# Kernel optimization log

Hardware: AMD Instinct MI355X
Metric: run time of the kernel (lower is better)

Reference implementation:

```python
import jax, jax.numpy as jnp
import numpy as np

B, A, T, D, H, NB, OUT = 64, 128, 6, 256, 512, 5, 401
ALPHA = 0.5
BETA = 0.5


def _lin_init(key, n_in, n_out, extra=()):
    bound = 1.0 / np.sqrt(n_in)
    kw, kb = jax.random.split(key)
    W = jax.random.uniform(kw, extra + (n_in, n_out), minval=-bound, maxval=bound, dtype=jnp.float32)
    b = jax.random.uniform(kb, extra + (n_out,), minval=-bound, maxval=bound, dtype=jnp.float32)
    return W, b


def setup_inputs() -> dict:
    key = jax.random.key(0)
    ks = jax.random.split(key, 8)
    stdv = 1.0 / np.sqrt(D)
    anchor = jax.random.uniform(ks[0], (1, 1, T, D), minval=-stdv, maxval=stdv, dtype=jnp.float32)
    sW1, sb1 = _lin_init(ks[1], D, D, (NB,))
    sW2, sb2 = _lin_init(ks[2], D, D, (NB,))
    cW1, cb1 = _lin_init(ks[3], D, D, (NB,))
    cW2, cb2 = _lin_init(ks[4], D, D, (NB,))
    dW1, db1 = _lin_init(ks[5], D, H)
    dW2, db2 = _lin_init(ks[6], H, OUT)
    final_embedding = jax.random.normal(ks[7], (B, A, D), dtype=jnp.float32)
    return {"final_embedding": final_embedding, "anchor": anchor,
            "sW1": sW1, "sb1": sb1, "sW2": sW2, "sb2": sb2,
            "cW1": cW1, "cb1": cb1, "cW2": cW2, "cb2": cb2,
            "dW1": dW1, "db1": db1, "dW2": dW2, "db2": db2}


def _mlp2(x, W1, b1, W2, b2):
    # 2-layer MLP (Linear -> ReLU -> Linear), applied to last dim
    return jax.nn.relu(x @ W1 + b1) @ W2 + b2


def reference(final_embedding, anchor, sW1, sb1, sW2, sb2, cW1, cb1, cW2, cb2, dW1, db1, dW2, db2):
    b, a = final_embedding.shape[:2]
    # s: [B, A, T, D] repeated anchors; c: [B, A, 1, D] context
    s = jnp.broadcast_to(anchor, (b, a, T, D))
    c = final_embedding[:, :, None, :]
    for i in range(NB):
        s_new = _mlp2(s, sW1[i], sb1[i], sW2[i], sb2[i])
        c_new = _mlp2(c, cW1[i], cb1[i], cW2[i], cb2[i])
        s_new = s_new * c_new                      # gate, broadcasts over T
        agg_c = jnp.max(s_new, axis=-2, keepdims=True)
        s = ALPHA * s + BETA * s_new               # sliding running mean
        c = ALPHA * c + BETA * agg_c
    # decoder MLP on trajectory embeddings s: [B, A, T, D]
    res = jax.nn.relu(s @ dW1 + db1) @ dW2 + db2   # [B, A, T, 401]
    coordinates = res[..., :160].reshape(b, a, T, 80, 2)
    av = res[..., 160:240].reshape(b, a, T, 80, 1)
    bv = res[..., 240:320].reshape(b, a, T, 80, 1)
    cv = res[..., 320:400].reshape(b, a, T, 80, 1)
    probas = res[..., -1]                          # [B, A, T]
    cov = jnp.concatenate([jnp.exp(av) * jnp.cosh(bv), jnp.sinh(bv),
                           jnp.sinh(bv), jnp.exp(-av) * jnp.cosh(bv)], axis=-1) * jnp.exp(cv)
    covariance_matrices = cov.reshape(b, a, T, 80, 2, 2)
    return (probas, coordinates, covariance_matrices)
```

## Files before the change

kernel.cpp:

```cpp
#include <hip/hip_runtime.h>
#include <math.h>


constexpr int Tn  = 6;
constexpr int Dn  = 256;
constexpr int Hn  = 512;
constexpr int NBn = 5;
constexpr int OUTn = 401;
constexpr int BA  = 8192;
constexpr int MR  = 49152;
constexpr float kAlpha = 0.5f;
constexpr float kBeta  = 0.5f;

typedef __bf16 bf16_8 __attribute__((ext_vector_type(8)));
typedef float  f32x4  __attribute__((ext_vector_type(4)));

__device__ __forceinline__ void async_copy16(const __bf16* g, __bf16* l) {
  __builtin_amdgcn_global_load_lds(
      (const __attribute__((address_space(1))) void*)g,
      (__attribute__((address_space(3))) void*)l, 16, 0, 0);
}

template<bool RELU, bool OUT_BF16>
__global__ __launch_bounds__(256) void gemm_mfma(
    const __bf16* __restrict__ A, const __bf16* __restrict__ BT,
    const float* __restrict__ bias, void* __restrict__ Cout,
    int M, int N, int K)
{
  __shared__ __align__(16) char smem[128 * 136 * 2];
  __bf16* As = (__bf16*)smem;
  __bf16* Bs = As + 128 * 32;

  const int tid = threadIdx.x;
  const int l   = tid & 63;
  const int w   = tid >> 6;
  const int wm  = w >> 1, wn = w & 1;

  const int GX = gridDim.x;
  const int total = GX * gridDim.y;
  const int L = blockIdx.y * GX + blockIdx.x;
  const int xcd = L & 7, pos = L >> 3;
  const int base = total >> 3, rem = total & 7;
  const int start = xcd * base + (xcd < rem ? xcd : rem);
  const int TL = start + pos;
  const int my = TL / GX;
  const int nx = TL - my * GX;
  const int m0 = my * 128;
  const int n0 = nx * 128;

  const int lrow = l >> 2;
  const int lk   = (l & 3) * 8;
  int ar0 = m0 + w * 32 + lrow;        if (ar0 > M - 1) ar0 = M - 1;
  int ar1 = m0 + w * 32 + 16 + lrow;   if (ar1 > M - 1) ar1 = M - 1;
  int br0 = n0 + w * 32 + lrow;        if (br0 > N - 1) br0 = N - 1;
  int br1 = n0 + w * 32 + 16 + lrow;   if (br1 > N - 1) br1 = N - 1;
  const __bf16* Ag0 = A  + (size_t)ar0 * K + lk;
  const __bf16* Ag1 = A  + (size_t)ar1 * K + lk;
  const __bf16* Bg0 = BT + (size_t)br0 * K + lk;
  const __bf16* Bg1 = BT + (size_t)br1 * K + lk;
  __bf16* Al = As + w * 1024;
  __bf16* Bl = Bs + w * 1024;

  f32x4 acc[4][4];
#pragma unroll
  for (int i = 0; i < 4; ++i)
#pragma unroll
    for (int j = 0; j < 4; ++j) acc[i][j] = (f32x4){0.f, 0.f, 0.f, 0.f};

  const __bf16* ap = As + (wm * 64 + (l & 15)) * 32 + (l >> 4) * 8;
  const __bf16* bp = Bs + (wn * 64 + (l & 15)) * 32 + (l >> 4) * 8;

  const int kIters = K >> 5;
  for (int kt = 0; kt < kIters; ++kt) {
    const int ko = kt * 32;
    async_copy16(Ag0 + ko, Al);
    async_copy16(Ag1 + ko, Al + 512);
    async_copy16(Bg0 + ko, Bl);
    async_copy16(Bg1 + ko, Bl + 512);
    __syncthreads();

    bf16_8 af[4], bf[4];
#pragma unroll
    for (int i = 0; i < 4; ++i) af[i] = *(const bf16_8*)(ap + i * 16 * 32);
#pragma unroll
    for (int j = 0; j < 4; ++j) bf[j] = *(const bf16_8*)(bp + j * 16 * 32);
#pragma unroll
    for (int i = 0; i < 4; ++i)
#pragma unroll
      for (int j = 0; j < 4; ++j)
        acc[i][j] = __builtin_amdgcn_mfma_f32_16x16x32_bf16(af[i], bf[j], acc[i][j], 0, 0, 0);
    __syncthreads();
  }

  const int colb = n0 + wn * 64 + (l & 15);
  const int rowb = m0 + wm * 64 + (l >> 4) * 4;

  if (OUT_BF16) {
    __bf16* Cs = (__bf16*)smem;
    const int lrb = wm * 64 + (l >> 4) * 4;
    const int lcb = wn * 64 + (l & 15);
#pragma unroll
    for (int j = 0; j < 4; ++j) {
      const float bj = bias[colb + j * 16];
#pragma unroll
      for (int i = 0; i < 4; ++i) {
#pragma unroll
        for (int r = 0; r < 4; ++r) {
          float v = acc[i][j][r] + bj;
          if (RELU) v = fmaxf(v, 0.0f);
          Cs[(lrb + i * 16 + r) * 136 + lcb + j * 16] = (__bf16)v;
        }
      }
    }
    __syncthreads();
    __bf16* Cg = (__bf16*)Cout;
#pragma unroll
    for (int it = 0; it < 8; ++it) {
      const int idx = it * 256 + tid;
      const int row = idx >> 4, c16 = idx & 15;
      const int gr = m0 + row;
      if (gr < M) {
        uint4 v = *(const uint4*)(Cs + row * 136 + c16 * 8);
        *(uint4*)(Cg + (size_t)gr * N + n0 + c16 * 8) = v;
      }
    }
  } else {
#pragma unroll
    for (int j = 0; j < 4; ++j) {
      const int gc = colb + j * 16;
      if (gc >= N) continue;
      const float bj = bias[gc];
#pragma unroll
      for (int i = 0; i < 4; ++i) {
        const int gr0 = rowb + i * 16;
#pragma unroll
        for (int r = 0; r < 4; ++r) {
          const int gr = gr0 + r;
          if (gr >= M) continue;
          float v = acc[i][j][r] + bj;
          if (RELU) v = fmaxf(v, 0.0f);
          ((float*)Cout)[(size_t)gr * N + gc] = v;
        }
      }
    }
  }
}

__global__ __launch_bounds__(256) void mlp2_c(
    const __bf16* __restrict__ X, const __bf16* __restrict__ W1T,
    const float* __restrict__ b1, const __bf16* __restrict__ W2T,
    const float* __restrict__ b2, __bf16* __restrict__ Out)
{
  __shared__ __align__(16) __bf16 Ast[32 * 32];
  __shared__ __align__(16) __bf16 Wst[256 * 32];
  __shared__ __align__(16) __bf16 Hb[8 * 32 * 32];
  const int tid = threadIdx.x, l = tid & 63, w = tid >> 6;
  const int m0 = blockIdx.x * 32;
  const int q4 = (l >> 4) * 4;

  f32x4 acc[2][4];
#pragma unroll
  for (int i = 0; i < 2; ++i)
#pragma unroll
    for (int j = 0; j < 4; ++j) acc[i][j] = (f32x4){0.f, 0.f, 0.f, 0.f};

  for (int kt = 0; kt < 8; ++kt) {
    const int ko = kt * 32;
    if (tid < 128) {
      const int ch = tid, row = ch >> 2, kk = (ch & 3) * 8;
      async_copy16(X + (size_t)(m0 + row) * Dn + ko + kk, Ast + ch * 8);
    }
#pragma unroll
    for (int r4 = 0; r4 < 4; ++r4) {
      const int ch = tid + r4 * 256, row = ch >> 2, kk = (ch & 3) * 8;
      async_copy16(W1T + (size_t)row * Dn + ko + kk, Wst + ch * 8);
    }
    __syncthreads();
    bf16_8 bf[4];
#pragma unroll
    for (int j = 0; j < 4; ++j)
      bf[j] = *(const bf16_8*)(Wst + (w * 64 + j * 16 + (l & 15)) * 32 + (l >> 4) * 8);
#pragma unroll
    for (int i = 0; i < 2; ++i) {
      bf16_8 af = *(const bf16_8*)(Ast + (i * 16 + (l & 15)) * 32 + (l >> 4) * 8);
#pragma unroll
      for (int j = 0; j < 4; ++j)
        acc[i][j] = __builtin_amdgcn_mfma_f32_16x16x32_bf16(af, bf[j], acc[i][j], 0, 0, 0);
    }
    __syncthreads();
  }

#pragma unroll
  for (int j = 0; j < 4; ++j) {
    const int col = w * 64 + j * 16 + (l & 15);
    const float bj = b1[col];
    __bf16* hc = Hb + (col >> 5) * 1024 + (col & 31);
#pragma unroll
    for (int i = 0; i < 2; ++i)
#pragma unroll
      for (int r = 0; r < 4; ++r) {
        const int row = i * 16 + q4 + r;
        hc[row * 32] = (__bf16)fmaxf(acc[i][j][r] + bj, 0.0f);
      }
  }
  __syncthreads();

#pragma unroll
  for (int i = 0; i < 2; ++i)
#pragma unroll
    for (int j = 0; j < 4; ++j) acc[i][j] = (f32x4){0.f, 0.f, 0.f, 0.f};
  for (int kt = 0; kt < 8; ++kt) {
    const int ko = kt * 32;
#pragma unroll
    for (int r4 = 0; r4 < 4; ++r4) {
      const int ch = tid + r4 * 256, row = ch >> 2, kk = (ch & 3) * 8;
      async_copy16(W2T + (size_t)row * Dn + ko + kk, Wst + ch * 8);
    }
    __syncthreads();
    bf16_8 bf[4];
#pragma unroll
    for (int j = 0; j < 4; ++j)
      bf[j] = *(const bf16_8*)(Wst + (w * 64 + j * 16 + (l & 15)) * 32 + (l >> 4) * 8);
#pragma unroll
    for (int i = 0; i < 2; ++i) {
      bf16_8 af = *(const bf16_8*)(Hb + kt * 1024 + (i * 16 + (l & 15)) * 32 + (l >> 4) * 8);
#pragma unroll
      for (int j = 0; j < 4; ++j)
        acc[i][j] = __builtin_amdgcn_mfma_f32_16x16x32_bf16(af, bf[j], acc[i][j], 0, 0, 0);
    }
    __syncthreads();
  }

#pragma unroll
  for (int j = 0; j < 4; ++j) {
    const int col = w * 64 + j * 16 + (l & 15);
    const float bj = b2[col];
#pragma unroll
    for (int i = 0; i < 2; ++i)
#pragma unroll
      for (int r = 0; r < 4; ++r) {
        const int row = i * 16 + q4 + r;
        Out[(size_t)(m0 + row) * Dn + col] = (__bf16)(acc[i][j][r] + bj);
      }
  }
}

__global__ __launch_bounds__(256) void mlp2_s(
    __bf16* __restrict__ S, const __bf16* __restrict__ W1T,
    const float* __restrict__ b1, const __bf16* __restrict__ W2T,
    const float* __restrict__ b2, const __bf16* __restrict__ Cnew,
    __bf16* __restrict__ C)
{
  __shared__ __align__(16) char smem[71680];
  __bf16* Ast  = (__bf16*)smem;
  __bf16* Wst  = (__bf16*)(smem + 6144);
  __bf16* Hb   = (__bf16*)(smem + 22528);
  __bf16* Snew = (__bf16*)smem;

  const int tid = threadIdx.x, l = tid & 63, w = tid >> 6;
  const int m0 = blockIdx.x * 96;
  const int q4 = (l >> 4) * 4;

  f32x4 acc[6][4];
#pragma unroll
  for (int i = 0; i < 6; ++i)
#pragma unroll
    for (int j = 0; j < 4; ++j) acc[i][j] = (f32x4){0.f, 0.f, 0.f, 0.f};

  for (int kt = 0; kt < 8; ++kt) {
    const int ko = kt * 32;
    { const int ch = tid, row = ch >> 2, kk = (ch & 3) * 8;
      async_copy16(S + (size_t)(m0 + row) * Dn + ko + kk, Ast + ch * 8); }
    if (tid < 128) {
      const int ch = 256 + tid, row = ch >> 2, kk = (ch & 3) * 8;
      async_copy16(S + (size_t)(m0 + row) * Dn + ko + kk, Ast + ch * 8);
    }
#pragma unroll
    for (int r4 = 0; r4 < 4; ++r4) {
      const int ch = tid + r4 * 256, row = ch >> 2, kk = (ch & 3) * 8;
      async_copy16(W1T + (size_t)row * Dn + ko + kk, Wst + ch * 8);
    }
    __syncthreads();
    bf16_8 bf[4];
#pragma unroll
    for (int j = 0; j < 4; ++j)
      bf[j] = *(const bf16_8*)(Wst + (w * 64 + j * 16 + (l & 15)) * 32 + (l >> 4) * 8);
#pragma unroll
    for (int i = 0; i < 6; ++i) {
      bf16_8 af = *(const bf16_8*)(Ast + (i * 16 + (l & 15)) * 32 + (l >> 4) * 8);
#pragma unroll
      for (int j = 0; j < 4; ++j)
        acc[i][j] = __builtin_amdgcn_mfma_f32_16x16x32_bf16(af, bf[j], acc[i][j], 0, 0, 0);
    }
    __syncthreads();
  }

#pragma unroll
  for (int j = 0; j < 4; ++j) {
    const int col = w * 64 + j * 16 + (l & 15);
    const float bj = b1[col];
    __bf16* hc = Hb + (col >> 5) * (96 * 32) + (col & 31);
#pragma unroll
    for (int i = 0; i < 6; ++i)
#pragma unroll
      for (int r = 0; r < 4; ++r) {
        const int row = i * 16 + q4 + r;
        hc[row * 32] = (__bf16)fmaxf(acc[i][j][r] + bj, 0.0f);
      }
  }
  __syncthreads();

#pragma unroll
  for (int i = 0; i < 6; ++i)
#pragma unroll
    for (int j = 0; j < 4; ++j) acc[i][j] = (f32x4){0.f, 0.f, 0.f, 0.f};
  for (int kt = 0; kt < 8; ++kt) {
    const int ko = kt * 32;
#pragma unroll
    for (int r4 = 0; r4 < 4; ++r4) {
      const int ch = tid + r4 * 256, row = ch >> 2, kk = (ch & 3) * 8;
      async_copy16(W2T + (size_t)row * Dn + ko + kk, Wst + ch * 8);
    }
    __syncthreads();
    bf16_8 bf[4];
#pragma unroll
    for (int j = 0; j < 4; ++j)
      bf[j] = *(const bf16_8*)(Wst + (w * 64 + j * 16 + (l & 15)) * 32 + (l >> 4) * 8);
#pragma unroll
    for (int i = 0; i < 6; ++i) {
      bf16_8 af = *(const bf16_8*)(Hb + kt * (96 * 32) + (i * 16 + (l & 15)) * 32 + (l >> 4) * 8);
#pragma unroll
      for (int j = 0; j < 4; ++j)
        acc[i][j] = __builtin_amdgcn_mfma_f32_16x16x32_bf16(af, bf[j], acc[i][j], 0, 0, 0);
    }
    __syncthreads();
  }

#pragma unroll
  for (int j = 0; j < 4; ++j) {
    const int col = w * 64 + j * 16 + (l & 15);
    const float bj = b2[col];
#pragma unroll
    for (int i = 0; i < 6; ++i)
#pragma unroll
      for (int r = 0; r < 4; ++r) {
        const int row = i * 16 + q4 + r;
        Snew[row * 264 + col] = (__bf16)(acc[i][j][r] + bj);
      }
  }
  __syncthreads();

#pragma unroll
  for (int p = 0; p < 2; ++p) {
    const int q = p * 256 + tid;
    const int ba = q >> 5, dg = (q & 31) * 8;
    const size_t gb = (size_t)(blockIdx.x * 16 + ba) * Dn + dg;
    bf16_8 cn8 = *(const bf16_8*)(Cnew + gb);
    float cn[8], m[8];
#pragma unroll
    for (int e = 0; e < 8; ++e) { cn[e] = (float)cn8[e]; m[e] = -3.402823466e38f; }
#pragma unroll
    for (int t = 0; t < Tn; ++t) {
      const int row = ba * 6 + t;
      bf16_8 sn8 = *(const bf16_8*)(Snew + row * 264 + dg);
      const size_t gs = (size_t)(m0 + row) * Dn + dg;
      bf16_8 s8 = *(const bf16_8*)(S + gs);
      bf16_8 o8;
#pragma unroll
      for (int e = 0; e < 8; ++e) {
        const float sn = (float)sn8[e] * cn[e];
        m[e] = fmaxf(m[e], sn);
        o8[e] = (__bf16)(kAlpha * (float)s8[e] + kBeta * sn);
      }
      *(bf16_8*)(S + gs) = o8;
    }
    bf16_8 c8 = *(const bf16_8*)(C + gb);
#pragma unroll
    for (int e = 0; e < 8; ++e)
      c8[e] = (__bf16)(kAlpha * (float)c8[e] + kBeta * m[e]);
    *(bf16_8*)(C + gb) = c8;
  }
}

__global__ __launch_bounds__(512, 4) void decoder2_fused(
    const __bf16* __restrict__ A, const __bf16* __restrict__ BT,
    const float* __restrict__ bias, float* __restrict__ out)
{
  __shared__ __align__(16) char smem[73728];
  float* mid = (float*)smem;

  const int tid = threadIdx.x, l = tid & 63, w = tid >> 6;
  const int m0 = blockIdx.x * 64;
  const int q4 = (l >> 4) * 4;

  f32x4 acc[4][4];
#pragma unroll
  for (int i = 0; i < 4; ++i)
#pragma unroll
    for (int j = 0; j < 4; ++j) acc[i][j] = (f32x4){0.f, 0.f, 0.f, 0.f};

  const __bf16* Ag = A + (size_t)(m0 + (tid >> 2)) * Hn + (tid & 3) * 8;
  const __bf16* Bg[4];
#pragma unroll
  for (int r4 = 0; r4 < 4; ++r4) {
    const int ch = tid + r4 * 512;
    int row = ch >> 2; if (row > 400) row = 400;
    Bg[r4] = BT + (size_t)row * Hn + (ch & 3) * 8;
  }

  auto stage = [&](int buf, int kt) {
    const int ko = kt * 32;
    __bf16* base = (__bf16*)(smem + buf * 36864);
    if (tid < 256) async_copy16(Ag + ko, base + tid * 8);
    __bf16* Bl = base + 64 * 32;
#pragma unroll
    for (int r4 = 0; r4 < 4; ++r4)
      async_copy16(Bg[r4] + ko, Bl + (size_t)(tid + r4 * 512) * 8);
  };

  stage(0, 0);
  __syncthreads();
  int cur = 0;
  for (int kt = 0; kt < 16; ++kt) {
    if (kt < 15) stage(cur ^ 1, kt + 1);
    const __bf16* Asl = (const __bf16*)(smem + cur * 36864);
    const __bf16* Bsl = Asl + 64 * 32;
    bf16_8 af[4], bf[4];
#pragma unroll
    for (int j = 0; j < 4; ++j)
      bf[j] = *(const bf16_8*)(Bsl + (w * 64 + j * 16 + (l & 15)) * 32 + (l >> 4) * 8);
#pragma unroll
    for (int i = 0; i < 4; ++i)
      af[i] = *(const bf16_8*)(Asl + (i * 16 + (l & 15)) * 32 + (l >> 4) * 8);
#pragma unroll
    for (int i = 0; i < 4; ++i)
#pragma unroll
      for (int j = 0; j < 4; ++j)
        acc[i][j] = __builtin_amdgcn_mfma_f32_16x16x32_bf16(af[i], bf[j], acc[i][j], 0, 0, 0);
    __syncthreads();
    cur ^= 1;
  }

  float* cov = out + MR + (size_t)MR * 160;
  const int gc = w * 64 + (l & 15);
#pragma unroll
  for (int sub = 0; sub < 2; ++sub) {
#pragma unroll
    for (int ih = 0; ih < 2; ++ih) {
      const int i = sub * 2 + ih;
#pragma unroll
      for (int j = 0; j < 4; ++j) {
        const int c = gc + j * 16;
        if (c > 400) continue;
        const float bj = bias[c];
#pragma unroll
        for (int r = 0; r < 4; ++r) {
          const int lr = ih * 16 + q4 + r;
          const int gr = m0 + sub * 32 + lr;
          const float v = acc[i][j][r] + bj;
          if (c < 160)      out[(size_t)MR + (size_t)gr * 160 + c] = v;
          else if (c < 400) mid[lr * 241 + (c - 160)] = v;
          else              out[gr] = v;
        }
      }
    }
    __syncthreads();
#pragma unroll
    for (int p = 0; p < 5; ++p) {
      const int q = p * 512 + tid;
      const int r32 = q / 80, j = q - r32 * 80;
      const int gr = m0 + sub * 32 + r32;
      const float av = mid[r32 * 241 + j];
      const float bv = mid[r32 * 241 + 80 + j];
      const float cv = mid[r32 * 241 + 160 + j];
      const float eb = __expf(bv), ebn = __expf(-bv);
      const float sh = 0.5f * (eb - ebn), ch = 0.5f * (eb + ebn);
      const float ea = __expf(av), ean = __expf(-av), ec = __expf(cv);
      f32x4 c4 = { ea * ch * ec, sh * ec, sh * ec, ean * ch * ec };
      *(f32x4*)(cov + (size_t)gr * 320 + 4 * j) = c4;
    }
    if (sub == 0) __syncthreads();
  }
}

__global__ __launch_bounds__(256) void transpose_bf16(
    const float* __restrict__ W, __bf16* __restrict__ WT, int K, int N)
{
  __shared__ float t[32][33];
  const int b  = blockIdx.z;
  const int tx = threadIdx.x, ty = threadIdx.y;
  const int k0 = blockIdx.y * 32, n0 = blockIdx.x * 32;
  const float* Wb  = W  + (size_t)b * K * N;
  __bf16*      WTb = WT + (size_t)b * N * K;
#pragma unroll
  for (int r = 0; r < 4; ++r) {
    int kk = k0 + ty + r * 8;
    if (kk < K && n0 + tx < N) t[ty + r * 8][tx] = Wb[(size_t)kk * N + n0 + tx];
  }
  __syncthreads();
#pragma unroll
  for (int r = 0; r < 4; ++r) {
    int nn = n0 + ty + r * 8;
    if (nn < N && k0 + tx < K)
      WTb[(size_t)nn * K + k0 + tx] = (__bf16)t[tx][ty + r * 8];
  }
}

__global__ __launch_bounds__(256) void convert_bf16(
    const float* __restrict__ in, __bf16* __restrict__ out, int n)
{
  int i = blockIdx.x * 256 + threadIdx.x;
  if (i < n) out[i] = (__bf16)in[i];
}

__global__ __launch_bounds__(256) void ew_update0(
    const float* __restrict__ anchor, const float* __restrict__ fe,
    const float* __restrict__ snewsm, const __bf16* __restrict__ cnew,
    __bf16* __restrict__ s, __bf16* __restrict__ c)
{
  int q = blockIdx.x * 256 + threadIdx.x;
  if (q >= BA * 32) return;
  int ba = q >> 5;
  int dg = (q & 31) * 8;
  bf16_8 cn8 = *(const bf16_8*)(cnew + (size_t)ba * Dn + dg);
  float cn[8], m[8];
#pragma unroll
  for (int e = 0; e < 8; ++e) { cn[e] = (float)cn8[e]; m[e] = -3.402823466e38f; }
  size_t base = (size_t)ba * Tn * Dn + dg;
#pragma unroll
  for (int t = 0; t < Tn; ++t) {
    bf16_8 o8;
#pragma unroll
    for (int e = 0; e < 8; ++e) {
      float sn = snewsm[t * Dn + dg + e] * cn[e];
      m[e] = fmaxf(m[e], sn);
      o8[e] = (__bf16)(kAlpha * anchor[t * Dn + dg + e] + kBeta * sn);
    }
    *(bf16_8*)(s + base + t * Dn) = o8;
  }
  bf16_8 c8;
#pragma unroll
  for (int e = 0; e < 8; ++e)
    c8[e] = (__bf16)(kAlpha * fe[(size_t)ba * Dn + dg + e] + kBeta * m[e]);
  *(bf16_8*)(c + (size_t)ba * Dn + dg) = c8;
}

extern "C" void kernel_launch(void* const* d_in, const int* in_sizes, int n_in,
                              void* d_out, int out_size, void* d_ws, size_t ws_size,
                              hipStream_t stream) {
  const float* fe     = (const float*)d_in[0];
  const float* anchor = (const float*)d_in[1];
  const float* sW1 = (const float*)d_in[2];
  const float* sb1 = (const float*)d_in[3];
  const float* sW2 = (const float*)d_in[4];
  const float* sb2 = (const float*)d_in[5];
  const float* cW1 = (const float*)d_in[6];
  const float* cb1 = (const float*)d_in[7];
  const float* cW2 = (const float*)d_in[8];
  const float* cb2 = (const float*)d_in[9];
  const float* dW1 = (const float*)d_in[10];
  const float* db1 = (const float*)d_in[11];
  const float* dW2 = (const float*)d_in[12];
  const float* db2 = (const float*)d_in[13];
  float* out = (float*)d_out;

  char* p = (char*)d_ws;
  __bf16* s_bf    = (__bf16*)(p + 0);
  __bf16* hd_bf   = (__bf16*)(p + 25165824);
  __bf16* c_bf    = (__bf16*)(p + 75497472);
  __bf16* cnew_bf = (__bf16*)(p + 79691776);
  __bf16* fe_bf   = (__bf16*)(p + 83886080);
  __bf16* sWT1    = (__bf16*)(p + 88080384);
  __bf16* sWT2    = (__bf16*)(p + 88735744);
  __bf16* cWT1    = (__bf16*)(p + 89391104);
  __bf16* cWT2    = (__bf16*)(p + 90046464);
  __bf16* dWT1    = (__bf16*)(p + 90701824);
  __bf16* dWT2    = (__bf16*)(p + 90963968);
  __bf16* anc_bf  = (__bf16*)(p + 91374592);
  __bf16* hsm_bf  = (__bf16*)(p + 91377664);
  float*  snewsm_f= (float* )(p + 91380736);

  auto gemm = [&](const __bf16* A, const __bf16* BT, const float* b, void* C,
                  int M, int N, int K, bool relu, bool outbf) {
    dim3 grid((N + 127) / 128, (M + 127) / 128);
    if (relu) {
      if (outbf) gemm_mfma<true,  true ><<<grid, 256, 0, stream>>>(A, BT, b, C, M, N, K);
      else       gemm_mfma<true,  false><<<grid, 256, 0, stream>>>(A, BT, b, C, M, N, K);
    } else {
      if (outbf) gemm_mfma<false, true ><<<grid, 256, 0, stream>>>(A, BT, b, C, M, N, K);
      else       gemm_mfma<false, false><<<grid, 256, 0, stream>>>(A, BT, b, C, M, N, K);
    }
  };

  {
    dim3 blk(32, 8);
    dim3 g88(8, 8, NBn);
    transpose_bf16<<<g88, blk, 0, stream>>>(sW1, sWT1, Dn, Dn);
    transpose_bf16<<<g88, blk, 0, stream>>>(sW2, sWT2, Dn, Dn);
    transpose_bf16<<<g88, blk, 0, stream>>>(cW1, cWT1, Dn, Dn);
    transpose_bf16<<<g88, blk, 0, stream>>>(cW2, cWT2, Dn, Dn);
    transpose_bf16<<<dim3(16, 8, 1), blk, 0, stream>>>(dW1, dWT1, Dn, Hn);
    transpose_bf16<<<dim3(13, 16, 1), blk, 0, stream>>>(dW2, dWT2, Hn, OUTn);
  }
  convert_bf16<<<(BA * Dn + 255) / 256, 256, 0, stream>>>(fe, fe_bf, BA * Dn);
  convert_bf16<<<(Tn * Dn + 255) / 256, 256, 0, stream>>>(anchor, anc_bf, Tn * Dn);

  const size_t WKK = (size_t)Dn * Dn;

  gemm(anc_bf, sWT1, sb1, hsm_bf,   Tn, Dn, Dn, true,  true);
  gemm(hsm_bf, sWT2, sb2, snewsm_f, Tn, Dn, Dn, false, false);
  mlp2_c<<<BA / 32, 256, 0, stream>>>(fe_bf, cWT1, cb1, cWT2, cb2, cnew_bf);
  ew_update0<<<(BA * 32 + 255) / 256, 256, 0, stream>>>(anchor, fe, snewsm_f,
                                                        cnew_bf, s_bf, c_bf);

  for (int i = 1; i < NBn; ++i) {
    mlp2_c<<<BA / 32, 256, 0, stream>>>(c_bf, cWT1 + i * WKK, cb1 + i * Dn,
                                        cWT2 + i * WKK, cb2 + i * Dn, cnew_bf);
    mlp2_s<<<MR / 96, 256, 0, stream>>>(s_bf, sWT1 + i * WKK, sb1 + i * Dn,
                                        sWT2 + i * WKK, sb2 + i * Dn,
                                        cnew_bf, c_bf);
  }

  gemm(s_bf, dWT1, db1, hd_bf, MR, Hn, Dn, true, true);
  decoder2_fused<<<MR / 64, 512, 0, stream>>>(hd_bf, dWT2, db2, out);
}
```

Measured before the change: 408.8 us.

## Double-buffer LDS tiles and widen MLP kernels to 512 threads

The generic GEMM and the layer-one loops of both block-MLP kernels now double-buffer their LDS tiles. The next K-slice is issued as an async global-to-LDS copy while the current one feeds the MFMAs, which also drops one barrier per iteration. mlp2_c and mlp2_s move from 256 to 512 threads with 8 waves, each computing a 32-column slice instead of 64. This halves per-thread accumulators and the share of weight loads each thread issues. The cost is more LDS per block, which may limit occupancy, and the layer-two loop of mlp2_s stays single-buffered.

Result: faster. 393.4 us (-3.8%).

```diff
diff --git a/kernel.cpp b/kernel.cpp
--- a/kernel.cpp
+++ b/kernel.cpp
@@ -27,9 +27,7 @@
     const float* __restrict__ bias, void* __restrict__ Cout,
     int M, int N, int K)
 {
-  __shared__ __align__(16) char smem[128 * 136 * 2];
-  __bf16* As = (__bf16*)smem;
-  __bf16* Bs = As + 128 * 32;
+  __shared__ __align__(16) char smem[34816];
 
   const int tid = threadIdx.x;
   const int l   = tid & 63;
@@ -58,8 +56,6 @@
   const __bf16* Ag1 = A  + (size_t)ar1 * K + lk;
   const __bf16* Bg0 = BT + (size_t)br0 * K + lk;
   const __bf16* Bg1 = BT + (size_t)br1 * K + lk;
-  __bf16* Al = As + w * 1024;
-  __bf16* Bl = Bs + w * 1024;
 
   f32x4 acc[4][4];
 #pragma unroll
@@ -67,17 +63,24 @@
 #pragma unroll
     for (int j = 0; j < 4; ++j) acc[i][j] = (f32x4){0.f, 0.f, 0.f, 0.f};
 
-  const __bf16* ap = As + (wm * 64 + (l & 15)) * 32 + (l >> 4) * 8;
-  const __bf16* bp = Bs + (wn * 64 + (l & 15)) * 32 + (l >> 4) * 8;
+  auto stage = [&](int buf, int ko) {
+    __bf16* As = (__bf16*)(smem + buf * 16384);
+    __bf16* Bs = As + 4096;
+    async_copy16(Ag0 + ko, As + w * 1024);
+    async_copy16(Ag1 + ko, As + w * 1024 + 512);
+    async_copy16(Bg0 + ko, Bs + w * 1024);
+    async_copy16(Bg1 + ko, Bs + w * 1024 + 512);
+  };
 
   const int kIters = K >> 5;
+  stage(0, 0);
+  __syncthreads();
   for (int kt = 0; kt < kIters; ++kt) {
-    const int ko = kt * 32;
-    async_copy16(Ag0 + ko, Al);
-    async_copy16(Ag1 + ko, Al + 512);
-    async_copy16(Bg0 + ko, Bl);
-    async_copy16(Bg1 + ko, Bl + 512);
-    __syncthreads();
+    if (kt + 1 < kIters) stage((kt + 1) & 1, (kt + 1) * 32);
+    const __bf16* As = (const __bf16*)(smem + (kt & 1) * 16384);
+    const __bf16* Bs = As + 4096;
+    const __bf16* ap = As + (wm * 64 + (l & 15)) * 32 + (l >> 4) * 8;
+    const __bf16* bp = Bs + (wn * 64 + (l & 15)) * 32 + (l >> 4) * 8;
 
     bf16_8 af[4], bf[4];
 #pragma unroll
@@ -146,53 +149,62 @@
   }
 }
 
-__global__ __launch_bounds__(256) void mlp2_c(
+__global__ __launch_bounds__(512) void mlp2_c(
     const __bf16* __restrict__ X, const __bf16* __restrict__ W1T,
     const float* __restrict__ b1, const __bf16* __restrict__ W2T,
     const float* __restrict__ b2, __bf16* __restrict__ Out)
 {
-  __shared__ __align__(16) __bf16 Ast[32 * 32];
-  __shared__ __align__(16) __bf16 Wst[256 * 32];
-  __shared__ __align__(16) __bf16 Hb[8 * 32 * 32];
+  __shared__ __align__(16) char smem[53248];
+  __bf16* Hb = (__bf16*)(smem + 36864);
+
   const int tid = threadIdx.x, l = tid & 63, w = tid >> 6;
   const int m0 = blockIdx.x * 32;
   const int q4 = (l >> 4) * 4;
 
-  f32x4 acc[2][4];
+  f32x4 acc[2][2];
 #pragma unroll
   for (int i = 0; i < 2; ++i)
 #pragma unroll
-    for (int j = 0; j < 4; ++j) acc[i][j] = (f32x4){0.f, 0.f, 0.f, 0.f};
-
+    for (int j = 0; j < 2; ++j) acc[i][j] = (f32x4){0.f, 0.f, 0.f, 0.f};
+
+  const __bf16* Xg = X + (size_t)(m0 + (tid >> 2)) * Dn + (tid & 3) * 8;
+
+  auto stageA = [&](int buf, int kt) {
+    if (tid < 128)
+      async_copy16(Xg + kt * 32, (__bf16*)(smem + buf * 2048) + tid * 8);
+  };
+  auto stageW = [&](const __bf16* WT, int buf, int kt) {
+    __bf16* Wstb = (__bf16*)(smem + 4096 + buf * 16384);
+#pragma unroll
+    for (int r2 = 0; r2 < 2; ++r2) {
+      const int ch = tid + r2 * 512, row = ch >> 2, kk = (ch & 3) * 8;
+      async_copy16(WT + (size_t)row * Dn + kt * 32 + kk, Wstb + ch * 8);
+    }
+  };
+
+  stageA(0, 0); stageW(W1T, 0, 0);
+  __syncthreads();
   for (int kt = 0; kt < 8; ++kt) {
-    const int ko = kt * 32;
-    if (tid < 128) {
-      const int ch = tid, row = ch >> 2, kk = (ch & 3) * 8;
-      async_copy16(X + (size_t)(m0 + row) * Dn + ko + kk, Ast + ch * 8);
-    }
-#pragma unroll
-    for (int r4 = 0; r4 < 4; ++r4) {
-      const int ch = tid + r4 * 256, row = ch >> 2, kk = (ch & 3) * 8;
-      async_copy16(W1T + (size_t)row * Dn + ko + kk, Wst + ch * 8);
-    }
-    __syncthreads();
-    bf16_8 bf[4];
-#pragma unroll
-    for (int j = 0; j < 4; ++j)
-      bf[j] = *(const bf16_8*)(Wst + (w * 64 + j * 16 + (l & 15)) * 32 + (l >> 4) * 8);
+    if (kt < 7) { stageA((kt + 1) & 1, kt + 1); stageW(W1T, (kt + 1) & 1, kt + 1); }
+    const __bf16* Astb = (const __bf16*)(smem + (kt & 1) * 2048);
+    const __bf16* Wstb = (const __bf16*)(smem + 4096 + (kt & 1) * 16384);
+    bf16_8 bf[2];
+#pragma unroll
+    for (int j = 0; j < 2; ++j)
+      bf[j] = *(const bf16_8*)(Wstb + (w * 32 + j * 16 + (l & 15)) * 32 + (l >> 4) * 8);
 #pragma unroll
     for (int i = 0; i < 2; ++i) {
-      bf16_8 af = *(const bf16_8*)(Ast + (i * 16 + (l & 15)) * 32 + (l >> 4) * 8);
-#pragma unroll
-      for (int j = 0; j < 4; ++j)
+      bf16_8 af = *(const bf16_8*)(Astb + (i * 16 + (l & 15)) * 32 + (l >> 4) * 8);
+#pragma unroll
+      for (int j = 0; j < 2; ++j)
         acc[i][j] = __builtin_amdgcn_mfma_f32_16x16x32_bf16(af, bf[j], acc[i][j], 0, 0, 0);
     }
     __syncthreads();
   }
 
 #pragma unroll
-  for (int j = 0; j < 4; ++j) {
-    const int col = w * 64 + j * 16 + (l & 15);
+  for (int j = 0; j < 2; ++j) {
+    const int col = w * 32 + j * 16 + (l & 15);
     const float bj = b1[col];
     __bf16* hc = Hb + (col >> 5) * 1024 + (col & 31);
 #pragma unroll
@@ -208,32 +220,29 @@
 #pragma unroll
   for (int i = 0; i < 2; ++i)
 #pragma unroll
-    for (int j = 0; j < 4; ++j) acc[i][j] = (f32x4){0.f, 0.f, 0.f, 0.f};
+    for (int j = 0; j < 2; ++j) acc[i][j] = (f32x4){0.f, 0.f, 0.f, 0.f};
+  stageW(W2T, 0, 0);
+  __syncthreads();
   for (int kt = 0; kt < 8; ++kt) {
-    const int ko = kt * 32;
-#pragma unroll
-    for (int r4 = 0; r4 < 4; ++r4) {
-      const int ch = tid + r4 * 256, row = ch >> 2, kk = (ch & 3) * 8;
-      async_copy16(W2T + (size_t)row * Dn + ko + kk, Wst + ch * 8);
-    }
-    __syncthreads();
-    bf16_8 bf[4];
-#pragma unroll
-    for (int j = 0; j < 4; ++j)
-      bf[j] = *(const bf16_8*)(Wst + (w * 64 + j * 16 + (l & 15)) * 32 + (l >> 4) * 8);
+    if (kt < 7) stageW(W2T, (kt + 1) & 1, kt + 1);
+    const __bf16* Wstb = (const __bf16*)(smem + 4096 + (kt & 1) * 16384);
+    bf16_8 bf[2];
+#pragma unroll
+    for (int j = 0; j < 2; ++j)
+      bf[j] = *(const bf16_8*)(Wstb + (w * 32 + j * 16 + (l & 15)) * 32 + (l >> 4) * 8);
 #pragma unroll
     for (int i = 0; i < 2; ++i) {
       bf16_8 af = *(const bf16_8*)(Hb + kt * 1024 + (i * 16 + (l & 15)) * 32 + (l >> 4) * 8);
 #pragma unroll
-      for (int j = 0; j < 4; ++j)
+      for (int j = 0; j < 2; ++j)
         acc[i][j] = __builtin_amdgcn_mfma_f32_16x16x32_bf16(af, bf[j], acc[i][j], 0, 0, 0);
     }
     __syncthreads();
   }
 
 #pragma unroll
-  for (int j = 0; j < 4; ++j) {
-    const int col = w * 64 + j * 16 + (l & 15);
+  for (int j = 0; j < 2; ++j) {
+    const int col = w * 32 + j * 16 + (l & 15);
     const float bj = b2[col];
 #pragma unroll
     for (int i = 0; i < 2; ++i)
@@ -245,15 +254,13 @@
   }
 }
 
-__global__ __launch_bounds__(256) void mlp2_s(
+__global__ __launch_bounds__(512) void mlp2_s(
     __bf16* __restrict__ S, const __bf16* __restrict__ W1T,
     const float* __restrict__ b1, const __bf16* __restrict__ W2T,
     const float* __restrict__ b2, const __bf16* __restrict__ Cnew,
     __bf16* __restrict__ C)
 {
   __shared__ __align__(16) char smem[71680];
-  __bf16* Ast  = (__bf16*)smem;
-  __bf16* Wst  = (__bf16*)(smem + 6144);
   __bf16* Hb   = (__bf16*)(smem + 22528);
   __bf16* Snew = (__bf16*)smem;
 
@@ -261,43 +268,48 @@
   const int m0 = blockIdx.x * 96;
   const int q4 = (l >> 4) * 4;
 
-  f32x4 acc[6][4];
+  f32x4 acc[6][2];
 #pragma unroll
   for (int i = 0; i < 6; ++i)
 #pragma unroll
-    for (int j = 0; j < 4; ++j) acc[i][j] = (f32x4){0.f, 0.f, 0.f, 0.f};
-
+    for (int j = 0; j < 2; ++j) acc[i][j] = (f32x4){0.f, 0.f, 0.f, 0.f};
+
+  const __bf16* Sg = S + (size_t)(m0 + (tid >> 2)) * Dn + (tid & 3) * 8;
+
+  auto stageL1 = [&](int buf, int kt) {
+    __bf16* Astb = (__bf16*)(smem + buf * 22528);
+    __bf16* Wstb = (__bf16*)(smem + buf * 22528 + 6144);
+    if (tid < 384) async_copy16(Sg + kt * 32, Astb + tid * 8);
+#pragma unroll
+    for (int r2 = 0; r2 < 2; ++r2) {
+      const int ch = tid + r2 * 512, row = ch >> 2, kk = (ch & 3) * 8;
+      async_copy16(W1T + (size_t)row * Dn + kt * 32 + kk, Wstb + ch * 8);
+    }
+  };
+
+  stageL1(0, 0);
+  __syncthreads();
   for (int kt = 0; kt < 8; ++kt) {
-    const int ko = kt * 32;
-    { const int ch = tid, row = ch >> 2, kk = (ch & 3) * 8;
-      async_copy16(S + (size_t)(m0 + row) * Dn + ko + kk, Ast + ch * 8); }
-    if (tid < 128) {
-      const int ch = 256 + tid, row = ch >> 2, kk = (ch & 3) * 8;
-      async_copy16(S + (size_t)(m0 + row) * Dn + ko + kk, Ast + ch * 8);
-    }
-#pragma unroll
-    for (int r4 = 0; r4 < 4; ++r4) {
-      const int ch = tid + r4 * 256, row = ch >> 2, kk = (ch & 3) * 8;
-      async_copy16(W1T + (size_t)row * Dn + ko + kk, Wst + ch * 8);
-    }
-    __syncthreads();
-    bf16_8 bf[4];
-#pragma unroll
-    for (int j = 0; j < 4; ++j)
-      bf[j] = *(const bf16_8*)(Wst + (w * 64 + j * 16 + (l & 15)) * 32 + (l >> 4) * 8);
+    if (kt < 7) stageL1((kt + 1) & 1, kt + 1);
+    const __bf16* Astb = (const __bf16*)(smem + (kt & 1) * 22528);
+    const __bf16* Wstb = Astb + 3072;
+    bf16_8 bf[2];
+#pragma unroll
+    for (int j = 0; j < 2; ++j)
+      bf[j] = *(const bf16_8*)(Wstb + (w * 32 + j * 16 + (l & 15)) * 32 + (l >> 4) * 8);
 #pragma unroll
     for (int i = 0; i < 6; ++i) {
-      bf16_8 af = *(const bf16_8*)(Ast + (i * 16 + (l & 15)) * 32 + (l >> 4) * 8);
-#pragma unroll
-      for (int j = 0; j < 4; ++j)
+      bf16_8 af = *(const bf16_8*)(Astb + (i * 16 + (l & 15)) * 32 + (l >> 4) * 8);
+#pragma unroll
+      for (int j = 0; j < 2; ++j)
         acc[i][j] = __builtin_amdgcn_mfma_f32_16x16x32_bf16(af, bf[j], acc[i][j], 0, 0, 0);
     }
     __syncthreads();
   }
 
 #pragma unroll
-  for (int j = 0; j < 4; ++j) {
-    const int col = w * 64 + j * 16 + (l & 15);
+  for (int j = 0; j < 2; ++j) {
+    const int col = w * 32 + j * 16 + (l & 15);
     const float bj = b1[col];
     __bf16* hc = Hb + (col >> 5) * (96 * 32) + (col & 31);
 #pragma unroll
@@ -313,32 +325,32 @@
 #pragma unroll
   for (int i = 0; i < 6; ++i)
 #pragma unroll
-    for (int j = 0; j < 4; ++j) acc[i][j] = (f32x4){0.f, 0.f, 0.f, 0.f};
+    for (int j = 0; j < 2; ++j) acc[i][j] = (f32x4){0.f, 0.f, 0.f, 0.f};
+  __bf16* Wst = (__bf16*)(smem + 6144);
   for (int kt = 0; kt < 8; ++kt) {
-    const int ko = kt * 32;
-#pragma unroll
-    for (int r4 = 0; r4 < 4; ++r4) {
-      const int ch = tid + r4 * 256, row = ch >> 2, kk = (ch & 3) * 8;
-      async_copy16(W2T + (size_t)row * Dn + ko + kk, Wst + ch * 8);
-    }
-    __syncthreads();
-    bf16_8 bf[4];
-#pragma unroll
-    for (int j = 0; j < 4; ++j)
-      bf[j] = *(const bf16_8*)(Wst + (w * 64 + j * 16 + (l & 15)) * 32 + (l >> 4) * 8);
+#pragma unroll
+    for (int r2 = 0; r2 < 2; ++r2) {
+      const int ch = tid + r2 * 512, row = ch >> 2, kk = (ch & 3) * 8;
+      async_copy16(W2T + (size_t)row * Dn + kt * 32 + kk, Wst + ch * 8);
+    }
+    __syncthreads();
+    bf16_8 bf[2];
+#pragma unroll
+    for (int j = 0; j < 2; ++j)
+      bf[j] = *(const bf16_8*)(Wst + (w * 32 + j * 16 + (l & 15)) * 32 + (l >> 4) * 8);
 #pragma unroll
     for (int i = 0; i < 6; ++i) {
       bf16_8 af = *(const bf16_8*)(Hb + kt * (96 * 32) + (i * 16 + (l & 15)) * 32 + (l >> 4) * 8);
 #pragma unroll
-      for (int j = 0; j < 4; ++j)
+      for (int j = 0; j < 2; ++j)
         acc[i][j] = __builtin_amdgcn_mfma_f32_16x16x32_bf16(af, bf[j], acc[i][j], 0, 0, 0);
     }
     __syncthreads();
   }
 
 #pragma unroll
-  for (int j = 0; j < 4; ++j) {
-    const int col = w * 64 + j * 16 + (l & 15);
+  for (int j = 0; j < 2; ++j) {
+    const int col = w * 32 + j * 16 + (l & 15);
     const float bj = b2[col];
 #pragma unroll
     for (int i = 0; i < 6; ++i)
@@ -350,10 +362,8 @@
   }
   __syncthreads();
 
-#pragma unroll
-  for (int p = 0; p < 2; ++p) {
-    const int q = p * 256 + tid;
-    const int ba = q >> 5, dg = (q & 31) * 8;
+  {
+    const int ba = tid >> 5, dg = (tid & 31) * 8;
     const size_t gb = (size_t)(blockIdx.x * 16 + ba) * Dn + dg;
     bf16_8 cn8 = *(const bf16_8*)(Cnew + gb);
     float cn[8], m[8];
@@ -609,14 +619,14 @@
 
   gemm(anc_bf, sWT1, sb1, hsm_bf,   Tn, Dn, Dn, true,  true);
   gemm(hsm_bf, sWT2, sb2, snewsm_f, Tn, Dn, Dn, false, false);
-  mlp2_c<<<BA / 32, 256, 0, stream>>>(fe_bf, cWT1, cb1, cWT2, cb2, cnew_bf);
+  mlp2_c<<<BA / 32, 512, 0, stream>>>(fe_bf, cWT1, cb1, cWT2, cb2, cnew_bf);
   ew_update0<<<(BA * 32 + 255) / 256, 256, 0, stream>>>(anchor, fe, snewsm_f,
                                                         cnew_bf, s_bf, c_bf);
 
   for (int i = 1; i < NBn; ++i) {
-    mlp2_c<<<BA / 32, 256, 0, stream>>>(c_bf, cWT1 + i * WKK, cb1 + i * Dn,
+    mlp2_c<<<BA / 32, 512, 0, stream>>>(c_bf, cWT1 + i * WKK, cb1 + i * Dn,
                                         cWT2 + i * WKK, cb2 + i * Dn, cnew_bf);
-    mlp2_s<<<MR / 96, 256, 0, stream>>>(s_bf, sWT1 + i * WKK, sb1 + i * Dn,
+    mlp2_s<<<MR / 96, 512, 0, stream>>>(s_bf, sWT1 + i * WKK, sb1 + i * Dn,
                                         sWT2 + i * WKK, sb2 + i * Dn,
                                         cnew_bf, c_bf);
   }
```
